# Performance work log

Measured on AMD Instinct MI355X. Metric: run time of the kernel, lower is better.

The kernel has to match this reference:

```python
import jax, jax.numpy as jnp
import numpy as np

G, NG, K, D = 64, 2048, 16, 256  # graphs, nodes/graph, eigvecs/graph, feature dim


def setup_inputs() -> dict:
    key = jax.random.key(0)
    k0, k1, k2, k3, k4 = jax.random.split(key, 5)
    x = jax.random.normal(k0, (G * NG, D), jnp.float32)
    # eigenvectors of per-graph Laplacians (values arbitrary for correctness baseline)
    eigvec = jax.random.normal(k1, (G * NG, K), jnp.float32) / np.float32(np.sqrt(NG))
    split_real = jnp.ones((D,), jnp.float32)
    split_imag = jnp.ones((D,), jnp.float32)
    spec_filter = jax.random.uniform(k2, (G, K, D), dtype=jnp.float32)
    W1 = jax.random.normal(k3, (D, D), jnp.float32) / np.float32(np.sqrt(D))
    W2 = jax.random.normal(k4, (D, D), jnp.float32) / np.float32(np.sqrt(D))
    factor_split = jnp.ones((D, 2), jnp.float32)
    return dict(x=x, eigvec=eigvec, split_real=split_real, split_imag=split_imag,
                spec_filter=spec_filter, W1=W1, W2=W2, factor_split=factor_split)


def _silu_norm(h):
    # SiLU gating: sigmoid of complex L2-norm over the spectral (k) axis, keepdim
    norm = jnp.sqrt(jnp.sum(h.real ** 2 + h.imag ** 2, axis=1, keepdims=True))
    return h * jax.nn.sigmoid(norm)


def reference(x, eigvec, split_real, split_imag, spec_filter, W1, W2, factor_split):
    # SpecFeatureTransformLayer (split variant): x -> complex
    xc = jax.lax.complex(split_real * x, split_imag * x)      # [N, D] complex64
    V = eigvec.reshape(G, NG, K)                              # block-diagonal eigvec basis
    xg = xc.reshape(G, NG, D)
    # eigvec^H @ x  (block-diag COO matmul, eigvecs real so conj is a no-op)
    x_spec = jnp.einsum('gnk,gnd->gkd', V, xg)                # [G, K, D] complex64
    x_spec = spec_filter * x_spec                             # learned spectral filter
    # silu_stack: MaybeComplexLinear (same real weight on real & imag) + norm-gated SiLU
    for W in (W1, W2):                                        # W: [out, in], y = x @ W^T
        h = jnp.einsum('gkd,ed->gke', x_spec, W)
        x_spec = _silu_norm(h)
    # project back to node domain: eigvec @ x_spec
    xn = jnp.einsum('gnk,gkd->gnd', V, x_spec).reshape(G * NG, D)
    # real/imag merge via factor_split
    out = xn.real * factor_split[:, 0] + xn.imag * factor_split[:, 1]
    return out + x                                            # node residual
```

## Files before the change

### kernel.cpp

```cpp
#include <hip/hip_runtime.h>
#include <math.h>

#define G  64
#define NG 2048
#define K  16
#define D  256
#define KD (K*D)
#define PROWS 128
#define NCHUNK (NG/PROWS)
#define WPF ((size_t)G * NCHUNK * KD)

typedef float v4f __attribute__((ext_vector_type(4)));

__global__ __launch_bounds__(256) void k_project(const float* __restrict__ x,
                                                 const float* __restrict__ eig,
                                                 float* __restrict__ WP) {
    __shared__ float sV[PROWS * K];
    __shared__ float red[2 * KD];
    const int b  = blockIdx.x;
    const int g  = b >> 4, c = b & 15;
    const int n0 = g * NG + c * PROWS;
    const int t  = threadIdx.x;
    const int d4 = t & 63;
    const int nq = t >> 6;

    {
        const float4* e4 = (const float4*)(eig + (size_t)n0 * K);
        float4* s4 = (float4*)sV;
        s4[t]       = e4[t];
        s4[t + 256] = e4[t + 256];
    }
    __syncthreads();

    float acc[K][4];
#pragma unroll
    for (int k = 0; k < K; ++k)
#pragma unroll
        for (int j = 0; j < 4; ++j) acc[k][j] = 0.f;

    const float4* x4 = (const float4*)x + ((size_t)n0 + nq * 32) * 64;
    const float* vbase = sV + nq * 32 * K;
#pragma unroll 4
    for (int n = 0; n < 32; ++n) {
        const float4 xv = x4[n * 64 + d4];
#pragma unroll
        for (int kq = 0; kq < 4; ++kq) {
            const float4 v = *(const float4*)&vbase[n * K + kq * 4];
            acc[kq*4+0][0] += v.x * xv.x; acc[kq*4+0][1] += v.x * xv.y;
            acc[kq*4+0][2] += v.x * xv.z; acc[kq*4+0][3] += v.x * xv.w;
            acc[kq*4+1][0] += v.y * xv.x; acc[kq*4+1][1] += v.y * xv.y;
            acc[kq*4+1][2] += v.y * xv.z; acc[kq*4+1][3] += v.y * xv.w;
            acc[kq*4+2][0] += v.z * xv.x; acc[kq*4+2][1] += v.z * xv.y;
            acc[kq*4+2][2] += v.z * xv.z; acc[kq*4+2][3] += v.z * xv.w;
            acc[kq*4+3][0] += v.w * xv.x; acc[kq*4+3][1] += v.w * xv.y;
            acc[kq*4+3][2] += v.w * xv.z; acc[kq*4+3][3] += v.w * xv.w;
        }
    }

    if (nq >= 2) {
#pragma unroll
        for (int k = 0; k < K; ++k)
            *(float4*)&red[(nq - 2) * KD + k * D + d4 * 4] =
                make_float4(acc[k][0], acc[k][1], acc[k][2], acc[k][3]);
    }
    __syncthreads();
    if (nq < 2) {
#pragma unroll
        for (int k = 0; k < K; ++k) {
            const float4 r = *(const float4*)&red[nq * KD + k * D + d4 * 4];
            acc[k][0] += r.x; acc[k][1] += r.y; acc[k][2] += r.z; acc[k][3] += r.w;
        }
    }
    __syncthreads();
    if (nq == 1) {
#pragma unroll
        for (int k = 0; k < K; ++k)
            *(float4*)&red[k * D + d4 * 4] =
                make_float4(acc[k][0], acc[k][1], acc[k][2], acc[k][3]);
    }
    __syncthreads();
    if (nq == 0) {
        float4* wp4 = (float4*)WP + (size_t)b * (KD / 4);
#pragma unroll
        for (int k = 0; k < K; ++k) {
            const float4 r = *(const float4*)&red[k * D + d4 * 4];
            wp4[k * 64 + d4] = make_float4(acc[k][0] + r.x, acc[k][1] + r.y,
                                           acc[k][2] + r.z, acc[k][3] + r.w);
        }
    }
}

__global__ __launch_bounds__(256) void k_reduce(const float* __restrict__ WP,
                                                const float* __restrict__ filt,
                                                const float* __restrict__ sr,
                                                const float* __restrict__ si,
                                                float* __restrict__ Xr,
                                                float* __restrict__ Xi) {
    const int b = blockIdx.x;
    const int g = b >> 2, q = b & 3;
    const int f = q * 256 + threadIdx.x;
    const float4* wp4 = (const float4*)WP + (size_t)g * NCHUNK * (KD / 4);
    float ax = 0.f, ay = 0.f, az = 0.f, aw = 0.f;
#pragma unroll
    for (int w = 0; w < NCHUNK; ++w) {
        const float4 p = wp4[(size_t)w * (KD / 4) + f];
        ax += p.x; ay += p.y; az += p.z; aw += p.w;
    }
    const float4 fl = ((const float4*)filt)[(size_t)g * (KD / 4) + f];
    const int d4 = f & 63;
    const float4 s0 = ((const float4*)sr)[d4];
    const float4 s1 = ((const float4*)si)[d4];
    float4 xr, xi;
    xr.x = ax * fl.x * s0.x; xr.y = ay * fl.y * s0.y;
    xr.z = az * fl.z * s0.z; xr.w = aw * fl.w * s0.w;
    xi.x = ax * fl.x * s1.x; xi.y = ay * fl.y * s1.y;
    xi.z = az * fl.z * s1.z; xi.w = aw * fl.w * s1.w;
    ((float4*)Xr)[(size_t)g * (KD / 4) + f] = xr;
    ((float4*)Xi)[(size_t)g * (KD / 4) + f] = xi;
}

template <int LAYER>
__global__ __launch_bounds__(256) void k_mlp(const float* __restrict__ Ar,
                                             const float* __restrict__ Ai,
                                             const float* __restrict__ W,
                                             const float* __restrict__ fs,
                                             float* __restrict__ o0,
                                             float* __restrict__ o1) {
    __shared__ float4 sW[32 * 64];
    __shared__ float  sNrm[8 * 32];
    __shared__ float  sSg[32];
    const int b     = blockIdx.x;
    const int g     = b >> 3;
    const int slice = b & 7;
    const int t     = threadIdx.x;

    {
        const float4* Wg = (const float4*)W + (size_t)slice * 32 * 64;
#pragma unroll
        for (int it = 0; it < 8; ++it) {
            const int idx = it * 256 + t;
            const int e = idx >> 6, ds = idx & 63;
            sW[e * 64 + (ds ^ (e & 7))] = Wg[idx];
        }
    }
    __syncthreads();

    const int el = t & 31;
    const int kg = t >> 5;
    const int e  = slice * 32 + el;
    const float* ar = Ar + (size_t)g * KD + (kg * 2) * D;
    const float* ai = Ai + (size_t)g * KD + (kg * 2) * D;

    float pr0 = 0.f, pr1 = 0.f, pi0 = 0.f, pi1 = 0.f;
#pragma unroll 8
    for (int ds = 0; ds < 64; ++ds) {
        const float4 w  = sW[el * 64 + (ds ^ (el & 7))];
        const float4 a0 = *(const float4*)&ar[ds * 4];
        const float4 a1 = *(const float4*)&ar[D + ds * 4];
        const float4 c0 = *(const float4*)&ai[ds * 4];
        const float4 c1 = *(const float4*)&ai[D + ds * 4];
        pr0 += w.x * a0.x + w.y * a0.y + w.z * a0.z + w.w * a0.w;
        pr1 += w.x * a1.x + w.y * a1.y + w.z * a1.z + w.w * a1.w;
        pi0 += w.x * c0.x + w.y * c0.y + w.z * c0.z + w.w * c0.w;
        pi1 += w.x * c1.x + w.y * c1.y + w.z * c1.z + w.w * c1.w;
    }

    sNrm[kg * 32 + el] = pr0 * pr0 + pi0 * pi0 + pr1 * pr1 + pi1 * pi1;
    __syncthreads();
    if (t < 32) {
        float nrm = 0.f;
#pragma unroll
        for (int w = 0; w < 8; ++w) nrm += sNrm[w * 32 + t];
        sSg[t] = 1.f / (1.f + expf(-sqrtf(nrm)));
    }
    __syncthreads();
    const float sg = sSg[el];

    float* base0 = o0 + (size_t)g * KD + (kg * 2) * D + e;
    if (LAYER == 1) {
        float* base1 = o1 + (size_t)g * KD + (kg * 2) * D + e;
        base0[0] = pr0 * sg; base0[D] = pr1 * sg;
        base1[0] = pi0 * sg; base1[D] = pi1 * sg;
    } else {
        const float f0 = fs[e * 2], f1 = fs[e * 2 + 1];
        base0[0] = (pr0 * f0 + pi0 * f1) * sg;
        base0[D] = (pr1 * f0 + pi1 * f1) * sg;
    }
}

__global__ __launch_bounds__(256) void k_back(const float* __restrict__ x,
                                              const float* __restrict__ eig,
                                              const float* __restrict__ z,
                                              float* __restrict__ out) {
    __shared__ float sV[PROWS * K];
    const int b  = blockIdx.x;
    const int g  = b >> 4, c = b & 15;
    const int n0 = g * NG + c * PROWS;
    const int t  = threadIdx.x;
    const int d4 = t & 63;
    const int nq = t >> 6;
    {
        const float4* e4 = (const float4*)(eig + (size_t)n0 * K);
        float4* s4 = (float4*)sV;
        s4[t]       = e4[t];
        s4[t + 256] = e4[t + 256];
    }
    float4 zr[K];
    const float4* z4 = (const float4*)z + (size_t)g * (KD / 4);
#pragma unroll
    for (int k = 0; k < K; ++k) zr[k] = z4[k * 64 + d4];
    __syncthreads();

    const float4* x4 = (const float4*)x + ((size_t)n0 + nq * 32) * 64;
    v4f* o4 = (v4f*)out + ((size_t)n0 + nq * 32) * 64;
    const float* vbase = sV + nq * 32 * K;
#pragma unroll 4
    for (int n = 0; n < 32; ++n) {
        float4 o = x4[n * 64 + d4];
#pragma unroll
        for (int kq = 0; kq < 4; ++kq) {
            const float4 v = *(const float4*)&vbase[n * K + kq * 4];
            o.x += v.x * zr[kq*4+0].x + v.y * zr[kq*4+1].x + v.z * zr[kq*4+2].x + v.w * zr[kq*4+3].x;
            o.y += v.x * zr[kq*4+0].y + v.y * zr[kq*4+1].y + v.z * zr[kq*4+2].y + v.w * zr[kq*4+3].y;
            o.z += v.x * zr[kq*4+0].z + v.y * zr[kq*4+1].z + v.z * zr[kq*4+2].z + v.w * zr[kq*4+3].z;
            o.w += v.x * zr[kq*4+0].w + v.y * zr[kq*4+1].w + v.z * zr[kq*4+2].w + v.w * zr[kq*4+3].w;
        }
        v4f ov; ov.x = o.x; ov.y = o.y; ov.z = o.z; ov.w = o.w;
        __builtin_nontemporal_store(ov, &o4[n * 64 + d4]);
    }
}

extern "C" void kernel_launch(void* const* d_in, const int* in_sizes, int n_in,
                              void* d_out, int out_size, void* d_ws, size_t ws_size,
                              hipStream_t stream) {
    const float* x    = (const float*)d_in[0];
    const float* eig  = (const float*)d_in[1];
    const float* sr   = (const float*)d_in[2];
    const float* si   = (const float*)d_in[3];
    const float* filt = (const float*)d_in[4];
    const float* W1   = (const float*)d_in[5];
    const float* W2   = (const float*)d_in[6];
    const float* fs   = (const float*)d_in[7];
    float* out = (float*)d_out;

    float* WP  = out;
    float* Xr  = out + WPF;
    float* Xi  = Xr + (size_t)G * KD;
    float* y1r = Xi + (size_t)G * KD;
    float* y1i = y1r + (size_t)G * KD;
    float* z   = (float*)d_ws;

    k_project<<<G * NCHUNK, 256, 0, stream>>>(x, eig, WP);
    k_reduce<<<G * 4, 256, 0, stream>>>(WP, filt, sr, si, Xr, Xi);
    k_mlp<1><<<G * 8, 256, 0, stream>>>(Xr, Xi, W1, nullptr, y1r, y1i);
    k_mlp<2><<<G * 8, 256, 0, stream>>>(y1r, y1i, W2, fs, z, nullptr);
    k_back<<<G * NCHUNK, 256, 0, stream>>>(x, eig, z, out);
}
```

Measured before the change: 316.6 us.

## Split projection work by eigvec group, stage MLP inputs in LDS, raise occupancy hints

```diff
diff --git a/kernel.cpp b/kernel.cpp
--- a/kernel.cpp
+++ b/kernel.cpp
@@ -12,17 +12,16 @@
 
 typedef float v4f __attribute__((ext_vector_type(4)));
 
-__global__ __launch_bounds__(256) void k_project(const float* __restrict__ x,
-                                                 const float* __restrict__ eig,
-                                                 float* __restrict__ WP) {
+__global__ __launch_bounds__(256, 6) void k_project(const float* __restrict__ x,
+                                                    const float* __restrict__ eig,
+                                                    float* __restrict__ WP) {
     __shared__ float sV[PROWS * K];
-    __shared__ float red[2 * KD];
     const int b  = blockIdx.x;
     const int g  = b >> 4, c = b & 15;
     const int n0 = g * NG + c * PROWS;
     const int t  = threadIdx.x;
     const int d4 = t & 63;
-    const int nq = t >> 6;
+    const int kq = t >> 6;
 
     {
         const float4* e4 = (const float4*)(eig + (size_t)n0 * K);
@@ -32,62 +31,34 @@
     }
     __syncthreads();
 
-    float acc[K][4];
-#pragma unroll
-    for (int k = 0; k < K; ++k)
-#pragma unroll
-        for (int j = 0; j < 4; ++j) acc[k][j] = 0.f;
-
-    const float4* x4 = (const float4*)x + ((size_t)n0 + nq * 32) * 64;
-    const float* vbase = sV + nq * 32 * K;
-#pragma unroll 4
-    for (int n = 0; n < 32; ++n) {
+    float acc[4][4];
+#pragma unroll
+    for (int j = 0; j < 4; ++j)
+#pragma unroll
+        for (int i = 0; i < 4; ++i) acc[j][i] = 0.f;
+
+    const float4* x4 = (const float4*)x + (size_t)n0 * 64;
+    const int rot = kq * 32;
+#pragma unroll 8
+    for (int i = 0; i < PROWS; ++i) {
+        const int n = (i + rot) & (PROWS - 1);
         const float4 xv = x4[n * 64 + d4];
-#pragma unroll
-        for (int kq = 0; kq < 4; ++kq) {
-            const float4 v = *(const float4*)&vbase[n * K + kq * 4];
-            acc[kq*4+0][0] += v.x * xv.x; acc[kq*4+0][1] += v.x * xv.y;
-            acc[kq*4+0][2] += v.x * xv.z; acc[kq*4+0][3] += v.x * xv.w;
-            acc[kq*4+1][0] += v.y * xv.x; acc[kq*4+1][1] += v.y * xv.y;
-            acc[kq*4+1][2] += v.y * xv.z; acc[kq*4+1][3] += v.y * xv.w;
-            acc[kq*4+2][0] += v.z * xv.x; acc[kq*4+2][1] += v.z * xv.y;
-            acc[kq*4+2][2] += v.z * xv.z; acc[kq*4+2][3] += v.z * xv.w;
-            acc[kq*4+3][0] += v.w * xv.x; acc[kq*4+3][1] += v.w * xv.y;
-            acc[kq*4+3][2] += v.w * xv.z; acc[kq*4+3][3] += v.w * xv.w;
-        }
-    }
-
-    if (nq >= 2) {
-#pragma unroll
-        for (int k = 0; k < K; ++k)
-            *(float4*)&red[(nq - 2) * KD + k * D + d4 * 4] =
-                make_float4(acc[k][0], acc[k][1], acc[k][2], acc[k][3]);
-    }
-    __syncthreads();
-    if (nq < 2) {
-#pragma unroll
-        for (int k = 0; k < K; ++k) {
-            const float4 r = *(const float4*)&red[nq * KD + k * D + d4 * 4];
-            acc[k][0] += r.x; acc[k][1] += r.y; acc[k][2] += r.z; acc[k][3] += r.w;
-        }
-    }
-    __syncthreads();
-    if (nq == 1) {
-#pragma unroll
-        for (int k = 0; k < K; ++k)
-            *(float4*)&red[k * D + d4 * 4] =
-                make_float4(acc[k][0], acc[k][1], acc[k][2], acc[k][3]);
-    }
-    __syncthreads();
-    if (nq == 0) {
-        float4* wp4 = (float4*)WP + (size_t)b * (KD / 4);
-#pragma unroll
-        for (int k = 0; k < K; ++k) {
-            const float4 r = *(const float4*)&red[k * D + d4 * 4];
-            wp4[k * 64 + d4] = make_float4(acc[k][0] + r.x, acc[k][1] + r.y,
-                                           acc[k][2] + r.z, acc[k][3] + r.w);
-        }
-    }
+        const float4 v  = *(const float4*)&sV[n * K + kq * 4];
+        acc[0][0] += v.x * xv.x; acc[0][1] += v.x * xv.y;
+        acc[0][2] += v.x * xv.z; acc[0][3] += v.x * xv.w;
+        acc[1][0] += v.y * xv.x; acc[1][1] += v.y * xv.y;
+        acc[1][2] += v.y * xv.z; acc[1][3] += v.y * xv.w;
+        acc[2][0] += v.z * xv.x; acc[2][1] += v.z * xv.y;
+        acc[2][2] += v.z * xv.z; acc[2][3] += v.z * xv.w;
+        acc[3][0] += v.w * xv.x; acc[3][1] += v.w * xv.y;
+        acc[3][2] += v.w * xv.z; acc[3][3] += v.w * xv.w;
+    }
+
+    float4* wp4 = (float4*)WP + (size_t)b * (KD / 4);
+#pragma unroll
+    for (int j = 0; j < 4; ++j)
+        wp4[(kq * 4 + j) * 64 + d4] =
+            make_float4(acc[j][0], acc[j][1], acc[j][2], acc[j][3]);
 }
 
 __global__ __launch_bounds__(256) void k_reduce(const float* __restrict__ WP,
@@ -127,6 +98,8 @@
                                              float* __restrict__ o0,
                                              float* __restrict__ o1) {
     __shared__ float4 sW[32 * 64];
+    __shared__ float4 sXr[K * 64];
+    __shared__ float4 sXi[K * 64];
     __shared__ float  sNrm[8 * 32];
     __shared__ float  sSg[32];
     const int b     = blockIdx.x;
@@ -142,23 +115,28 @@
             const int e = idx >> 6, ds = idx & 63;
             sW[e * 64 + (ds ^ (e & 7))] = Wg[idx];
         }
+        const float4* ar4 = (const float4*)Ar + (size_t)g * (KD / 4);
+        const float4* ai4 = (const float4*)Ai + (size_t)g * (KD / 4);
+#pragma unroll
+        for (int it = 0; it < 4; ++it) {
+            sXr[it * 256 + t] = ar4[it * 256 + t];
+            sXi[it * 256 + t] = ai4[it * 256 + t];
+        }
     }
     __syncthreads();
 
     const int el = t & 31;
     const int kg = t >> 5;
     const int e  = slice * 32 + el;
-    const float* ar = Ar + (size_t)g * KD + (kg * 2) * D;
-    const float* ai = Ai + (size_t)g * KD + (kg * 2) * D;
 
     float pr0 = 0.f, pr1 = 0.f, pi0 = 0.f, pi1 = 0.f;
 #pragma unroll 8
     for (int ds = 0; ds < 64; ++ds) {
         const float4 w  = sW[el * 64 + (ds ^ (el & 7))];
-        const float4 a0 = *(const float4*)&ar[ds * 4];
-        const float4 a1 = *(const float4*)&ar[D + ds * 4];
-        const float4 c0 = *(const float4*)&ai[ds * 4];
-        const float4 c1 = *(const float4*)&ai[D + ds * 4];
+        const float4 a0 = sXr[(kg * 2) * 64 + ds];
+        const float4 a1 = sXr[(kg * 2 + 1) * 64 + ds];
+        const float4 c0 = sXi[(kg * 2) * 64 + ds];
+        const float4 c1 = sXi[(kg * 2 + 1) * 64 + ds];
         pr0 += w.x * a0.x + w.y * a0.y + w.z * a0.z + w.w * a0.w;
         pr1 += w.x * a1.x + w.y * a1.y + w.z * a1.z + w.w * a1.w;
         pi0 += w.x * c0.x + w.y * c0.y + w.z * c0.z + w.w * c0.w;
@@ -188,10 +166,10 @@
     }
 }
 
-__global__ __launch_bounds__(256) void k_back(const float* __restrict__ x,
-                                              const float* __restrict__ eig,
-                                              const float* __restrict__ z,
-                                              float* __restrict__ out) {
+__global__ __launch_bounds__(256, 4) void k_back(const float* __restrict__ x,
+                                                 const float* __restrict__ eig,
+                                                 const float* __restrict__ z,
+                                                 float* __restrict__ out) {
     __shared__ float sV[PROWS * K];
     const int b  = blockIdx.x;
     const int g  = b >> 4, c = b & 15;
@@ -214,7 +192,7 @@
     const float4* x4 = (const float4*)x + ((size_t)n0 + nq * 32) * 64;
     v4f* o4 = (v4f*)out + ((size_t)n0 + nq * 32) * 64;
     const float* vbase = sV + nq * 32 * K;
-#pragma unroll 4
+#pragma unroll 8
     for (int n = 0; n < 32; ++n) {
         float4 o = x4[n * 64 + d4];
 #pragma unroll
```

Result: slower. 346.7 us (+9.5%).
